# Kernel optimization log

Measured on AMD Instinct MI355X. Metric: run time of the kernel, lower is better.

Reference implementation:

```python
import jax, jax.numpy as jnp
import numpy as np

N, M, D, K = 32768, 8192, 384, 9


def setup_inputs() -> dict:
    key = jax.random.key(0)
    k1, k2 = jax.random.split(key)
    return {
        "embedding": jax.random.normal(k1, (N, D), dtype=jnp.float32),
        "memory_bank": jax.random.normal(k2, (M, D), dtype=jnp.float32),
        "n_neighbors": K,
    }


def reference(embedding, memory_bank, n_neighbors):
    x_norm = jnp.sum(embedding * embedding, axis=-1, keepdims=True)      # [N, 1]
    y_norm = jnp.sum(memory_bank * memory_bank, axis=-1, keepdims=True)  # [M, 1]
    d2 = x_norm - 2.0 * jnp.matmul(embedding, memory_bank.T) + y_norm.T  # [N, M]
    dist = jnp.sqrt(jnp.maximum(d2, 0.0))
    # topk smallest along dim 1 (patch_scores, indices discarded)
    neg_top, _ = jax.lax.top_k(-dist, n_neighbors)
    patch_scores = -neg_top  # [N, K], ascending distances
    return patch_scores
```

## Files before the change

### kernel.cpp

```cpp
#include <hip/hip_runtime.h>
#include <hip/hip_bf16.h>

#define N_ROWS 32768
#define M_ROWS 8192
#define D_DIM  384
#define K_NB   9
#define BN     32
#define BM     128
#define NMQ    8
#define MQ     (M_ROWS / NMQ)
#define TILES  (MQ / BN)
#define KS     3

#define QSCALE (1.0f / 2048.0f)
#define YOFF   0.125f
#define QSTEPF (2048.0f / 65535.0f)
#define QOFFB  256.0f
#define M2S    (-2.0f / 2048.0f)
#define BIGF   3.0e38f

#define BUFSZ  12288
#define YS_OFF 24576

typedef __attribute__((ext_vector_type(4))) int      i32x4;
typedef __attribute__((ext_vector_type(8))) int      i32x8;
typedef __attribute__((ext_vector_type(4))) float    f32x4;
typedef __attribute__((ext_vector_type(2))) unsigned u32x2;

#define GLDS(SRC, DST)                                                       \
  __builtin_amdgcn_global_load_lds(                                          \
      (const __attribute__((address_space(1))) void*)(SRC),                  \
      (__attribute__((address_space(3))) void*)(DST), 16, 0, 0)

#define MF(AF, B, C)                                                         \
  __builtin_amdgcn_mfma_scale_f32_16x16x128_f8f6f4(                          \
      (AF), (B), (C), 0, 0, 0, 0x7F7F7F7F, 0, 0x7F7F7F7F)

__global__ __launch_bounds__(256) void FAPM_prep8(
    const float* __restrict__ emb, const float* __restrict__ mem,
    unsigned* __restrict__ A8, unsigned* __restrict__ B8,
    float* __restrict__ xn, float* __restrict__ yn) {
  const int lane = threadIdx.x & 63;
  const int row  = blockIdx.x * 4 + (threadIdx.x >> 6);
  const float* src;
  unsigned* dst;
  float* nptr;
  if (row < N_ROWS) {
    src = emb + (size_t)row * D_DIM; dst = A8 + (size_t)row * 96; nptr = xn + row;
  } else {
    int r = row - N_ROWS;
    src = mem + (size_t)r * D_DIM; dst = B8 + (size_t)r * 96; nptr = yn + r;
  }
  float s = 0.f;
  {
    int dw = lane;
    f32x4 v = *(const f32x4*)(src + dw * 4);
    s += v.x * v.x + v.y * v.y + v.z * v.z + v.w * v.w;
    int pk = __builtin_amdgcn_cvt_pk_fp8_f32(v.x, v.y, 0, false);
    pk = __builtin_amdgcn_cvt_pk_fp8_f32(v.z, v.w, pk, true);
    dst[dw] = (unsigned)pk;
  }
  if (lane < 32) {
    int dw = lane + 64;
    f32x4 v = *(const f32x4*)(src + dw * 4);
    s += v.x * v.x + v.y * v.y + v.z * v.z + v.w * v.w;
    int pk = __builtin_amdgcn_cvt_pk_fp8_f32(v.x, v.y, 0, false);
    pk = __builtin_amdgcn_cvt_pk_fp8_f32(v.z, v.w, pk, true);
    dst[dw] = (unsigned)pk;
  }
#pragma unroll
  for (int dd = 1; dd < 64; dd <<= 1) s += __shfl_xor(s, dd);
  if (lane == 0) *nptr = s;
}

__device__ __forceinline__ unsigned pkmin(unsigned a, unsigned b) {
  unsigned d;
  asm("v_pk_min_u16 %0, %1, %2" : "=v"(d) : "v"(a), "v"(b));
  return d;
}
__device__ __forceinline__ unsigned pkmax(unsigned a, unsigned b) {
  unsigned d;
  asm("v_pk_max_u16 %0, %1, %2" : "=v"(d) : "v"(a), "v"(b));
  return d;
}

__device__ __forceinline__ void merge16i(unsigned t[9], float* dst, int sub) {
  for (int s = 0; s < K_NB; ++s) {
    unsigned m  = t[0];
    int      ml = sub;
#pragma unroll
    for (int dd = 1; dd < 16; dd <<= 1) {
      unsigned ov = (unsigned)__shfl_xor((int)m, dd);
      int      ol = __shfl_xor(ml, dd);
      bool take = (ov < m) || (ov == m && ol < ml);
      m  = take ? ov : m;
      ml = take ? ol : ml;
    }
    if (sub == ml) {
#pragma unroll
      for (int j = 0; j < 8; ++j) t[j] = t[j + 1];
      t[8] = 0xFFFFu;
    }
    if (sub == 0) dst[s] = (float)m * QSTEPF - QOFFB;
  }
}

#define STAGE_B(GB, DSTO)                                                    \
  if ((w & 1) == 0) {                                                        \
    GLDS((GB), LDS + (DSTO));                                                \
    GLDS((GB) + 16, LDS + (DSTO) + 1024);                                    \
    GLDS((GB) + 128, LDS + (DSTO) + 2048);                                   \
  } else {                                                                   \
    GLDS((GB) + 144, LDS + (DSTO));                                          \
    GLDS((GB) + 256, LDS + (DSTO) + 1024);                                   \
    GLDS((GB) + 272, LDS + (DSTO) + 2048);                                   \
  }

__global__ __launch_bounds__(256, 4) void FAPM_fused(
    const unsigned char* __restrict__ A8, const unsigned char* __restrict__ B8,
    const float* __restrict__ yn, float* __restrict__ part) {
  __shared__ __attribute__((aligned(128))) unsigned char LDS[26624];
  const int tid  = threadIdx.x;
  const int lane = tid & 63;
  const int w    = tid >> 6;
  const int sub  = lane & 15;
  const int grp  = lane >> 4;
  const int bx   = blockIdx.x;
  const int mq   = bx & (NMQ - 1);
  const int row0 = (bx >> 3) * BM;
  const int colbase = mq * MQ;

  if (tid < 128) {
    const float* yp = yn + colbase + tid * 8;
    f32x4 v0 = *(const f32x4*)yp;
    f32x4 v1 = *(const f32x4*)(yp + 4);
    float a0 = fmaf(v0.x, QSCALE, YOFF), a1 = fmaf(v0.y, QSCALE, YOFF);
    float a2 = fmaf(v0.z, QSCALE, YOFF), a3 = fmaf(v0.w, QSCALE, YOFF);
    float a4 = fmaf(v1.x, QSCALE, YOFF), a5 = fmaf(v1.y, QSCALE, YOFF);
    float a6 = fmaf(v1.z, QSCALE, YOFF), a7 = fmaf(v1.w, QSCALE, YOFF);
    unsigned q0, q1, q2, q3;
    asm("v_cvt_pknorm_u16_f32 %0, %1, %2" : "=v"(q0) : "v"(a0), "v"(a1));
    asm("v_cvt_pknorm_u16_f32 %0, %1, %2" : "=v"(q1) : "v"(a2), "v"(a3));
    asm("v_cvt_pknorm_u16_f32 %0, %1, %2" : "=v"(q2) : "v"(a4), "v"(a5));
    asm("v_cvt_pknorm_u16_f32 %0, %1, %2" : "=v"(q3) : "v"(a6), "v"(a7));
    *(u32x2*)(&LDS[YS_OFF + tid * 16]) = (u32x2){q0, q1};
    *(u32x2*)(&LDS[YS_OFF + tid * 16 + 8]) = (u32x2){q2, q3};
  }

  i32x8 af[2][KS];

#pragma unroll
  for (int r = 0; r < 2; ++r) {
    const unsigned char* asrc =
        A8 + (size_t)(row0 + r * 64 + w * 16 + sub) * D_DIM + grp * 32;
#pragma unroll
    for (int ks = 0; ks < KS; ++ks)
#pragma unroll
      for (int h = 0; h < 2; ++h)
        GLDS(asrc + ks * 128 + h * 16, LDS + (w * 6 + ks * 2 + h) * 1024);
    asm volatile("s_waitcnt vmcnt(0)" ::: "memory");
    __syncthreads();
    if ((w >> 1) == r) {
#pragma unroll
      for (int rbl = 0; rbl < 2; ++rbl) {
        const int g = (w & 1) * 2 + rbl;
#pragma unroll
        for (int ks = 0; ks < KS; ++ks) {
          const unsigned char* p = LDS + (g * 6 + ks * 2) * 1024 + lane * 16;
          *(i32x4*)&af[rbl][ks] = *(const i32x4*)p;
          *((i32x4*)&af[rbl][ks] + 1) = *(const i32x4*)(p + 1024);
        }
      }
    }
    __syncthreads();
  }

  const unsigned char* bbase =
      B8 + (size_t)(colbase + (w >> 1) * 16 + sub) * D_DIM + grp * 32;
  const int bdst = w * 3 * 1024;

  STAGE_B(bbase, bdst);
  STAGE_B(bbase + BUFSZ, BUFSZ + bdst);
  bbase += 2 * BUFSZ;

  unsigned tkp[4][9];
#pragma unroll
  for (int i = 0; i < 4; ++i)
#pragma unroll
    for (int j = 0; j < 9; ++j) tkp[i][j] = 0xFFFFFFFFu;

  for (int t = 0; t < TILES; ++t) {
    const int bufo = (t & 1) * BUFSZ;
    if (t + 1 < TILES) asm volatile("s_waitcnt vmcnt(3)" ::: "memory");
    else               asm volatile("s_waitcnt vmcnt(0)" ::: "memory");
    __builtin_amdgcn_s_barrier();

    const unsigned char* br = LDS + bufo + lane * 16;
#pragma unroll
    for (int cb = 0; cb < 2; ++cb) {
      unsigned yu = *(const unsigned short*)(
          &LDS[YS_OFF + ((t * BN + cb * 16 + sub) << 1)]);
      float ysv = (float)yu * (1.0f / 65535.0f);

      f32x4 acc0 = {0.f, 0.f, 0.f, 0.f}, acc1 = {0.f, 0.f, 0.f, 0.f};
      __builtin_amdgcn_s_setprio(1);
#pragma unroll
      for (int ks = 0; ks < KS; ++ks) {
        i32x8 b;
        const unsigned char* p = br + cb * 6144 + ks * 2048;
        *(i32x4*)&b = *(const i32x4*)p;
        *((i32x4*)&b + 1) = *(const i32x4*)(p + 1024);
        acc0 = MF(af[0][ks], b, acc0);
        acc1 = MF(af[1][ks], b, acc1);
      }
      __builtin_amdgcn_s_setprio(0);

#pragma unroll
      for (int i = 0; i < 4; ++i) {
        float d2a = fmaf(acc0[i], M2S, ysv);
        float d2b = fmaf(acc1[i], M2S, ysv);
        unsigned dp;
        asm("v_cvt_pknorm_u16_f32 %0, %1, %2" : "=v"(dp) : "v"(d2a), "v"(d2b));
#pragma unroll
        for (int j = 8; j >= 1; --j)
          tkp[i][j] = pkmin(tkp[i][j], pkmax(dp, tkp[i][j - 1]));
        tkp[i][0] = pkmin(tkp[i][0], dp);
      }
    }
    __builtin_amdgcn_s_barrier();

    if (t + 2 < TILES) {
      STAGE_B(bbase, bufo + bdst);
      bbase += BUFSZ;
    }
  }

  float* pbase = part + (size_t)mq * N_ROWS * K_NB;
#pragma unroll
  for (int i = 0; i < 4; ++i) {
    unsigned ta[9], tb[9];
#pragma unroll
    for (int j = 0; j < 9; ++j) { ta[j] = tkp[i][j] & 0xFFFFu; tb[j] = tkp[i][j] >> 16; }
    int rowA = row0 + w * 32 + grp * 4 + i;
    merge16i(ta, pbase + (size_t)rowA * K_NB, sub);
    merge16i(tb, pbase + (size_t)(rowA + 16) * K_NB, sub);
  }
}

__device__ __forceinline__ void merge4lists(float l[4][9], float o[9]) {
#pragma unroll
  for (int s = 0; s < K_NB; ++s) {
    float m = fminf(fminf(l[0][0], l[1][0]), fminf(l[2][0], l[3][0]));
    o[s] = m;
    bool t0 = (l[0][0] == m);
    bool t1 = (l[1][0] == m) && !t0;
    bool t2 = (l[2][0] == m) && !t0 && !t1;
    bool t3 = !(t0 || t1 || t2);
#pragma unroll
    for (int j = 0; j < 8; ++j) {
      l[0][j] = t0 ? l[0][j + 1] : l[0][j];
      l[1][j] = t1 ? l[1][j + 1] : l[1][j];
      l[2][j] = t2 ? l[2][j + 1] : l[2][j];
      l[3][j] = t3 ? l[3][j + 1] : l[3][j];
    }
    l[0][8] = t0 ? BIGF : l[0][8];
    l[1][8] = t1 ? BIGF : l[1][8];
    l[2][8] = t2 ? BIGF : l[2][8];
    l[3][8] = t3 ? BIGF : l[3][8];
  }
}

__global__ __launch_bounds__(256) void FAPM_merge8(
    const float* __restrict__ part, const float* __restrict__ xn,
    float* __restrict__ out) {
  const int r = blockIdx.x * 256 + threadIdx.x;
  const float xr = xn[r];
  float l[4][9], a[9], b[9];
#pragma unroll
  for (int q = 0; q < 4; ++q)
#pragma unroll
    for (int j = 0; j < 9; ++j)
      l[q][j] = part[(size_t)q * N_ROWS * K_NB + (size_t)r * K_NB + j];
  merge4lists(l, a);
#pragma unroll
  for (int q = 0; q < 4; ++q)
#pragma unroll
    for (int j = 0; j < 9; ++j)
      l[q][j] = part[(size_t)(q + 4) * N_ROWS * K_NB + (size_t)r * K_NB + j];
  merge4lists(l, b);
#pragma unroll
  for (int s = 0; s < K_NB; ++s) {
    bool ta = a[0] <= b[0];
    float m = ta ? a[0] : b[0];
    out[(size_t)r * K_NB + s] = sqrtf(fmaxf(m + xr, 0.f));
#pragma unroll
    for (int j = 0; j < 8; ++j) {
      float an = a[j + 1], bn = b[j + 1];
      a[j] = ta ? an : a[j];
      b[j] = ta ? b[j] : bn;
    }
    a[8] = ta ? BIGF : a[8];
    b[8] = ta ? b[8] : BIGF;
  }
}

extern "C" void kernel_launch(void* const* d_in, const int* in_sizes, int n_in,
                              void* d_out, int out_size, void* d_ws, size_t ws_size,
                              hipStream_t stream) {
  const float* emb = (const float*)d_in[0];
  const float* mem = (const float*)d_in[1];
  float* out = (float*)d_out;
  char* ws = (char*)d_ws;
  size_t offA = 0;
  size_t offB = offA + (size_t)N_ROWS * D_DIM;
  size_t offX = offB + (size_t)M_ROWS * D_DIM;
  size_t offY = offX + (size_t)N_ROWS * 4;
  size_t offP = offY + (size_t)M_ROWS * 4;
  unsigned char* A8 = (unsigned char*)(ws + offA);
  unsigned char* B8 = (unsigned char*)(ws + offB);
  float* xn = (float*)(ws + offX);
  float* yn = (float*)(ws + offY);
  float* part = (float*)(ws + offP);

  FAPM_prep8<<<(N_ROWS + M_ROWS) / 4, 256, 0, stream>>>(
      emb, mem, (unsigned*)A8, (unsigned*)B8, xn, yn);
  FAPM_fused<<<(N_ROWS / BM) * NMQ, 256, 0, stream>>>(A8, B8, yn, part);
  FAPM_merge8<<<N_ROWS / 256, 256, 0, stream>>>(part, xn, out);
}
```

Before: 194.6 us.

## Halve column splits and software-pipeline MFMA with delayed top-k insertion

Reduces the memory-bank column split from 8 to 4 quarters, so each block scans twice as many tiles, fewer partial top-k lists are written, and the final merge handles 4 lists instead of 8. Inside the tile loop, the top-k insertion for the previous 16-column chunk is interleaved with the MFMA accumulation of the next chunk, so VALU selection work can overlap matrix instructions. The y-norm staging now uses all 256 threads with 128-bit LDS writes, and LDS grows to hold the larger column slice. Occupancy drops to 3 blocks per CU and register pressure rises from carrying the extra accumulators, and the grid has half as many blocks.

```diff
diff --git a/kernel.cpp b/kernel.cpp
--- a/kernel.cpp
+++ b/kernel.cpp
@@ -7,7 +7,7 @@
 #define K_NB   9
 #define BN     32
 #define BM     128
-#define NMQ    8
+#define NMQ    4
 #define MQ     (M_ROWS / NMQ)
 #define TILES  (MQ / BN)
 #define KS     3
@@ -25,7 +25,7 @@
 typedef __attribute__((ext_vector_type(4))) int      i32x4;
 typedef __attribute__((ext_vector_type(8))) int      i32x8;
 typedef __attribute__((ext_vector_type(4))) float    f32x4;
-typedef __attribute__((ext_vector_type(2))) unsigned u32x2;
+typedef __attribute__((ext_vector_type(4))) unsigned u32x4;
 
 #define GLDS(SRC, DST)                                                       \
   __builtin_amdgcn_global_load_lds(                                          \
@@ -105,6 +105,21 @@
   }
 }
 
+__device__ __forceinline__ void topk_ins(const f32x4& a0, const f32x4& a1,
+                                         float ysv, unsigned tkp[4][9]) {
+#pragma unroll
+  for (int i = 0; i < 4; ++i) {
+    float d2a = fmaf(a0[i], M2S, ysv);
+    float d2b = fmaf(a1[i], M2S, ysv);
+    unsigned dp;
+    asm("v_cvt_pknorm_u16_f32 %0, %1, %2" : "=v"(dp) : "v"(d2a), "v"(d2b));
+#pragma unroll
+    for (int j = 8; j >= 1; --j)
+      tkp[i][j] = pkmin(tkp[i][j], pkmax(dp, tkp[i][j - 1]));
+    tkp[i][0] = pkmin(tkp[i][0], dp);
+  }
+}
+
 #define STAGE_B(GB, DSTO)                                                    \
   if ((w & 1) == 0) {                                                        \
     GLDS((GB), LDS + (DSTO));                                                \
@@ -116,10 +131,10 @@
     GLDS((GB) + 272, LDS + (DSTO) + 2048);                                   \
   }
 
-__global__ __launch_bounds__(256, 4) void FAPM_fused(
+__global__ __launch_bounds__(256, 3) void FAPM_fused(
     const unsigned char* __restrict__ A8, const unsigned char* __restrict__ B8,
     const float* __restrict__ yn, float* __restrict__ part) {
-  __shared__ __attribute__((aligned(128))) unsigned char LDS[26624];
+  __shared__ __attribute__((aligned(128))) unsigned char LDS[28672];
   const int tid  = threadIdx.x;
   const int lane = tid & 63;
   const int w    = tid >> 6;
@@ -127,10 +142,10 @@
   const int grp  = lane >> 4;
   const int bx   = blockIdx.x;
   const int mq   = bx & (NMQ - 1);
-  const int row0 = (bx >> 3) * BM;
+  const int row0 = (bx >> 2) * BM;
   const int colbase = mq * MQ;
 
-  if (tid < 128) {
+  {
     const float* yp = yn + colbase + tid * 8;
     f32x4 v0 = *(const f32x4*)yp;
     f32x4 v1 = *(const f32x4*)(yp + 4);
@@ -143,8 +158,7 @@
     asm("v_cvt_pknorm_u16_f32 %0, %1, %2" : "=v"(q1) : "v"(a2), "v"(a3));
     asm("v_cvt_pknorm_u16_f32 %0, %1, %2" : "=v"(q2) : "v"(a4), "v"(a5));
     asm("v_cvt_pknorm_u16_f32 %0, %1, %2" : "=v"(q3) : "v"(a6), "v"(a7));
-    *(u32x2*)(&LDS[YS_OFF + tid * 16]) = (u32x2){q0, q1};
-    *(u32x2*)(&LDS[YS_OFF + tid * 16 + 8]) = (u32x2){q2, q3};
+    *(u32x4*)(&LDS[YS_OFF + tid * 16]) = (u32x4){q0, q1, q2, q3};
   }
 
   i32x8 af[2][KS];
@@ -189,6 +203,10 @@
 #pragma unroll
     for (int j = 0; j < 9; ++j) tkp[i][j] = 0xFFFFFFFFu;
 
+  f32x4 pA0 = {-BIGF, -BIGF, -BIGF, -BIGF};
+  f32x4 pA1 = {-BIGF, -BIGF, -BIGF, -BIGF};
+  float pYs = 0.f;
+
   for (int t = 0; t < TILES; ++t) {
     const int bufo = (t & 1) * BUFSZ;
     if (t + 1 < TILES) asm volatile("s_waitcnt vmcnt(3)" ::: "memory");
@@ -196,37 +214,36 @@
     __builtin_amdgcn_s_barrier();
 
     const unsigned char* br = LDS + bufo + lane * 16;
-#pragma unroll
-    for (int cb = 0; cb < 2; ++cb) {
-      unsigned yu = *(const unsigned short*)(
-          &LDS[YS_OFF + ((t * BN + cb * 16 + sub) << 1)]);
-      float ysv = (float)yu * (1.0f / 65535.0f);
-
-      f32x4 acc0 = {0.f, 0.f, 0.f, 0.f}, acc1 = {0.f, 0.f, 0.f, 0.f};
-      __builtin_amdgcn_s_setprio(1);
-#pragma unroll
-      for (int ks = 0; ks < KS; ++ks) {
-        i32x8 b;
-        const unsigned char* p = br + cb * 6144 + ks * 2048;
-        *(i32x4*)&b = *(const i32x4*)p;
-        *((i32x4*)&b + 1) = *(const i32x4*)(p + 1024);
-        acc0 = MF(af[0][ks], b, acc0);
-        acc1 = MF(af[1][ks], b, acc1);
-      }
-      __builtin_amdgcn_s_setprio(0);
-
-#pragma unroll
-      for (int i = 0; i < 4; ++i) {
-        float d2a = fmaf(acc0[i], M2S, ysv);
-        float d2b = fmaf(acc1[i], M2S, ysv);
-        unsigned dp;
-        asm("v_cvt_pknorm_u16_f32 %0, %1, %2" : "=v"(dp) : "v"(d2a), "v"(d2b));
-#pragma unroll
-        for (int j = 8; j >= 1; --j)
-          tkp[i][j] = pkmin(tkp[i][j], pkmax(dp, tkp[i][j - 1]));
-        tkp[i][0] = pkmin(tkp[i][0], dp);
-      }
-    }
+    unsigned yu0 = *(const unsigned short*)(&LDS[YS_OFF + ((t * BN + sub) << 1)]);
+    unsigned yu1 = *(const unsigned short*)(&LDS[YS_OFF + ((t * BN + 16 + sub) << 1)]);
+    float ys0 = (float)yu0 * (1.0f / 65535.0f);
+    float ys1 = (float)yu1 * (1.0f / 65535.0f);
+
+    f32x4 a0 = {0.f, 0.f, 0.f, 0.f}, a1 = {0.f, 0.f, 0.f, 0.f};
+#pragma unroll
+    for (int ks = 0; ks < KS; ++ks) {
+      i32x8 b;
+      const unsigned char* p = br + ks * 2048;
+      *(i32x4*)&b = *(const i32x4*)p;
+      *((i32x4*)&b + 1) = *(const i32x4*)(p + 1024);
+      a0 = MF(af[0][ks], b, a0);
+      a1 = MF(af[1][ks], b, a1);
+    }
+    topk_ins(pA0, pA1, pYs, tkp);
+
+    f32x4 c0 = {0.f, 0.f, 0.f, 0.f}, c1 = {0.f, 0.f, 0.f, 0.f};
+#pragma unroll
+    for (int ks = 0; ks < KS; ++ks) {
+      i32x8 b;
+      const unsigned char* p = br + 6144 + ks * 2048;
+      *(i32x4*)&b = *(const i32x4*)p;
+      *((i32x4*)&b + 1) = *(const i32x4*)(p + 1024);
+      c0 = MF(af[0][ks], b, c0);
+      c1 = MF(af[1][ks], b, c1);
+    }
+    topk_ins(a0, a1, ys0, tkp);
+    pA0 = c0; pA1 = c1; pYs = ys1;
+
     __builtin_amdgcn_s_barrier();
 
     if (t + 2 < TILES) {
@@ -234,6 +251,7 @@
       bbase += BUFSZ;
     }
   }
+  topk_ins(pA0, pA1, pYs, tkp);
 
   float* pbase = part + (size_t)mq * N_ROWS * K_NB;
 #pragma unroll
@@ -247,11 +265,21 @@
   }
 }
 
-__device__ __forceinline__ void merge4lists(float l[4][9], float o[9]) {
+__global__ __launch_bounds__(256) void FAPM_merge4(
+    const float* __restrict__ part, const float* __restrict__ xn,
+    float* __restrict__ out) {
+  const int r = blockIdx.x * 256 + threadIdx.x;
+  const float xr = xn[r];
+  float l[4][9];
+#pragma unroll
+  for (int q = 0; q < 4; ++q)
+#pragma unroll
+    for (int j = 0; j < 9; ++j)
+      l[q][j] = part[(size_t)q * N_ROWS * K_NB + (size_t)r * K_NB + j];
 #pragma unroll
   for (int s = 0; s < K_NB; ++s) {
     float m = fminf(fminf(l[0][0], l[1][0]), fminf(l[2][0], l[3][0]));
-    o[s] = m;
+    out[(size_t)r * K_NB + s] = sqrtf(fmaxf(m + xr, 0.f));
     bool t0 = (l[0][0] == m);
     bool t1 = (l[1][0] == m) && !t0;
     bool t2 = (l[2][0] == m) && !t0 && !t1;
@@ -267,40 +295,6 @@
     l[1][8] = t1 ? BIGF : l[1][8];
     l[2][8] = t2 ? BIGF : l[2][8];
     l[3][8] = t3 ? BIGF : l[3][8];
-  }
-}
-
-__global__ __launch_bounds__(256) void FAPM_merge8(
-    const float* __restrict__ part, const float* __restrict__ xn,
-    float* __restrict__ out) {
-  const int r = blockIdx.x * 256 + threadIdx.x;
-  const float xr = xn[r];
-  float l[4][9], a[9], b[9];
-#pragma unroll
-  for (int q = 0; q < 4; ++q)
-#pragma unroll
-    for (int j = 0; j < 9; ++j)
-      l[q][j] = part[(size_t)q * N_ROWS * K_NB + (size_t)r * K_NB + j];
-  merge4lists(l, a);
-#pragma unroll
-  for (int q = 0; q < 4; ++q)
-#pragma unroll
-    for (int j = 0; j < 9; ++j)
-      l[q][j] = part[(size_t)(q + 4) * N_ROWS * K_NB + (size_t)r * K_NB + j];
-  merge4lists(l, b);
-#pragma unroll
-  for (int s = 0; s < K_NB; ++s) {
-    bool ta = a[0] <= b[0];
-    float m = ta ? a[0] : b[0];
-    out[(size_t)r * K_NB + s] = sqrtf(fmaxf(m + xr, 0.f));
-#pragma unroll
-    for (int j = 0; j < 8; ++j) {
-      float an = a[j + 1], bn = b[j + 1];
-      a[j] = ta ? an : a[j];
-      b[j] = ta ? b[j] : bn;
-    }
-    a[8] = ta ? BIGF : a[8];
-    b[8] = ta ? b[8] : BIGF;
   }
 }
 
@@ -325,5 +319,5 @@
   FAPM_prep8<<<(N_ROWS + M_ROWS) / 4, 256, 0, stream>>>(
       emb, mem, (unsigned*)A8, (unsigned*)B8, xn, yn);
   FAPM_fused<<<(N_ROWS / BM) * NMQ, 256, 0, stream>>>(A8, B8, yn, part);
-  FAPM_merge8<<<N_ROWS / 256, 256, 0, stream>>>(part, xn, out);
-}
+  FAPM_merge4<<<N_ROWS / 256, 256, 0, stream>>>(part, xn, out);
+}
```

After: 183.0 us. 1.06x faster.
